# Optimization experiments

Measured on AMD Instinct MI355X. Metric: run time of the kernel, lower is better.

Reference implementation:

```python
import jax, jax.numpy as jnp
import numpy as np

B, C, N, D, K, M, E, G = 2, 64, 16384, 3, 128, 1, 262144, 3


def setup_inputs() -> dict:
    key = jax.random.key(0)
    ks = jax.random.split(key, 15)
    scale = 1.0 / (C * C)
    return {
        "x": jax.random.normal(ks[0], (B, C, N), jnp.float32),
        "nodes": jax.random.uniform(ks[1], (B, N, D), jnp.float32),
        "node_weights": jax.random.uniform(ks[2], (B, N, M), jnp.float32),
        "geo": jax.random.normal(ks[3], (B, G, N), jnp.float32),
        "directed_edges": jax.random.randint(ks[4], (B, E, 2), 0, N, jnp.int32),
        "edge_gradient_weights": 0.1 * jax.random.normal(ks[5], (B, E, D), jnp.float32),
        "modes": jax.random.normal(ks[6], (K, D, M), jnp.float32),
        "weights_c": scale * jax.random.uniform(ks[7], (C, C, K, M), jnp.float32),
        "weights_s": scale * jax.random.uniform(ks[8], (C, C, K, M), jnp.float32),
        "weights_0": scale * jax.random.uniform(ks[9], (C, C, 1, M), jnp.float32),
        "W": jax.random.normal(ks[10], (C, C), jnp.float32) / np.sqrt(C),
        "gw": jax.random.normal(ks[11], (C, C * D), jnp.float32) / np.sqrt(C * D),
        "geo_wx": jax.random.normal(ks[12], (C, G), jnp.float32) / np.sqrt(G),
        "wx": jax.random.normal(ks[13], (C, C), jnp.float32) / np.sqrt(C),
        "w2": jax.random.normal(ks[14], (C, C), jnp.float32) / np.sqrt(C),
    }


def reference(x, nodes, node_weights, geo, directed_edges, edge_gradient_weights,
              modes, weights_c, weights_s, weights_0, W, gw, geo_wx, wx, w2):
    # ---- Fourier bases: cos(kx), sin(kx), 1 -------------------------------
    temp = jnp.einsum('bxd,kdw->bxkw', nodes, modes)          # [B,N,K,M]
    bases_c, bases_s = jnp.cos(temp), jnp.sin(temp)
    b, n = temp.shape[0], temp.shape[1]
    bases_0 = jnp.ones((b, n, 1, temp.shape[3]), temp.dtype)
    nw = node_weights[:, :, None, :]                          # quadrature weights
    wb_c, wb_s, wb_0 = bases_c * nw, bases_s * nw, bases_0 * nw

    # ---- Spectral convolution (non-uniform Fourier neural layer) ----------
    x_c = jnp.einsum('bix,bxkw->bikw', x, wb_c)
    x_s = -jnp.einsum('bix,bxkw->bikw', x, wb_s)
    x_0 = jnp.einsum('bix,bxkw->bikw', x, wb_0)
    f_c = jnp.einsum('bikw,iokw->bokw', x_c, weights_c) - jnp.einsum('bikw,iokw->bokw', x_s, weights_s)
    f_s = jnp.einsum('bikw,iokw->bokw', x_s, weights_c) + jnp.einsum('bikw,iokw->bokw', x_c, weights_s)
    f_0 = jnp.einsum('bikw,iokw->bokw', x_0, weights_0)
    x1 = (jnp.einsum('bokw,bxkw->box', f_0, bases_0)
          + 2.0 * jnp.einsum('bokw,bxkw->box', f_c, bases_c)
          - 2.0 * jnp.einsum('bokw,bxkw->box', f_s, bases_s))

    # ---- Pointwise linear W ----------------------------------------------
    x2 = jnp.einsum('oi,bix->box', W, x)

    # ---- Least-squares gradient via edge gather + scatter-add -------------
    fT = jnp.transpose(x, (0, 2, 1))                          # [B,N,C]
    tgt, src = directed_edges[..., 0], directed_edges[..., 1]  # [B,E]
    f_src = jnp.take_along_axis(fT, src[:, :, None], axis=1)   # [B,E,C]
    f_tgt = jnp.take_along_axis(fT, tgt[:, :, None], axis=1)
    df = f_src - f_tgt
    # message[b,e,c,d] = w[b,e,d] * df[b,e,c], flattened c-major -> [B,E,C*D]
    msg = (df[..., :, None] * edge_gradient_weights[..., None, :]).reshape(b, tgt.shape[1], -1)
    gradf = jnp.zeros((b, n, msg.shape[-1]), msg.dtype).at[jnp.arange(b)[:, None], tgt].add(msg)
    x3 = jnp.einsum('og,bng->bon', gw, gradf)                  # [B,C,N]

    # ---- Geo embedding: w2 @ (softsign(geo_wx@geo) * (wx@x)) --------------
    h = jax.nn.soft_sign(jnp.einsum('og,bgx->box', geo_wx, geo)) * jnp.einsum('oi,bix->box', wx, x)
    x4 = jnp.einsum('oi,bix->box', w2, h)

    return jax.nn.gelu(x1 + x2 + x3 + x4, approximate=False)
```

## Files before the change

kernel.cpp:

```cpp
#include <hip/hip_runtime.h>
#include <hip/hip_fp16.h>
#include <math.h>

#define BB 2
#define CC 64
#define NN 16384
#define DD 3
#define KK 128
#define EE 262144
#define GG 3
#define PP 128
#define LL (NN/PP)
#define KTOT 576

typedef short bf16x8 __attribute__((ext_vector_type(8)));
typedef float f32x4  __attribute__((ext_vector_type(4)));

__device__ __forceinline__ short f2bf(float f) {
    unsigned u = __float_as_uint(f);
    u += 0x7FFF + ((u >> 16) & 1);
    return (short)(u >> 16);
}
__device__ __forceinline__ float bf2f(unsigned short u) {
    return __uint_as_float(((unsigned)u) << 16);
}

constexpr size_t OFF_XB   = 0;
constexpr size_t OFF_PC   = OFF_XB   + (size_t)BB*NN*32;
constexpr size_t OFF_PS   = OFF_PC   + (size_t)BB*PP*CC*KK;
constexpr size_t OFF_BIN4 = OFF_PC;
constexpr size_t OFF_AC   = OFF_PS   + (size_t)BB*PP*CC*KK;
constexpr size_t OFF_AS   = OFF_AC   + (size_t)BB*CC*KK;
constexpr size_t OFF_F0   = OFF_AS   + (size_t)BB*CC*KK;
constexpr size_t OFF_X0   = OFF_F0   + (size_t)BB*CC;
constexpr size_t OFF_CNT  = OFF_X0   + (size_t)BB*CC;
constexpr size_t OFF_OFFS = OFF_CNT  + (size_t)BB*NN;
constexpr size_t OFF_RANK = OFF_OFFS + (size_t)BB*NN;
constexpr size_t OFF_GRB  = OFF_RANK + (size_t)BB*EE;
constexpr size_t OFF_APAN = OFF_GRB  + (size_t)BB*NN*96;
constexpr size_t OFF_GWXT = OFF_APAN + (size_t)BB*KTOT*CC/2;

#define S_A0 (BB*(NN/64))
#define S_A1 (S_A0 + BB*CC)
#define S_A2 (S_A1 + (BB*EE)/256)
#define S_A3 (S_A2 + 48)
#define S_A4 (S_A3 + BB*PP*4)
__global__ void __launch_bounds__(256) k1(const float* __restrict__ x,
                                          const float* __restrict__ nwt,
                                          const int* __restrict__ edges,
                                          const float* __restrict__ W,
                                          const float* __restrict__ gw,
                                          const float* __restrict__ geo_wx,
                                          const float* __restrict__ w2,
                                          const float* __restrict__ nodes,
                                          const float* __restrict__ modes,
                                          unsigned short* __restrict__ xB,
                                          float* __restrict__ x0,
                                          int* __restrict__ counts,
                                          int* __restrict__ rank,
                                          float* __restrict__ gwxT,
                                          short* __restrict__ ApanB,
                                          float* __restrict__ pc,
                                          float* __restrict__ ps) {
    int blk = blockIdx.x;
    int tid = threadIdx.x;
    __shared__ __align__(16) char smem[36864];
    if (blk < S_A0) {
        float (*tile)[65] = (float (*)[65])smem;
        int b = blk / (NN/64);
        int n0 = (blk % (NN/64)) * 64;
        int c = tid & 63, r4 = tid >> 6;
        for (int rr = 0; rr < 16; rr++) {
            int i = r4*16 + rr;
            tile[i][c] = x[((size_t)b*CC + i)*NN + n0 + c];
        }
        __syncthreads();
        for (int rr = 0; rr < 16; rr++) {
            int nn = r4*16 + rr;
            xB[((size_t)b*NN + n0 + nn)*64 + c] = (unsigned short)f2bf(tile[c][nn]);
        }
    } else if (blk < S_A1) {
        float* red = (float*)smem;
        int bi = blk - S_A0;
        int b = bi >> 6, i = bi & 63;
        const float4* __restrict__ xr = (const float4*)&x[((size_t)b*CC + i)*NN];
        const float4* __restrict__ wr = (const float4*)&nwt[(size_t)b*NN];
        float s = 0.f;
        for (int t = tid; t < NN/4; t += 256) {
            float4 xv = xr[t];
            float4 wv = wr[t];
            s += xv.x*wv.x + xv.y*wv.y + xv.z*wv.z + xv.w*wv.w;
        }
        red[tid] = s;
        __syncthreads();
        for (int off = 128; off > 0; off >>= 1) {
            if (tid < off) red[tid] += red[tid+off];
            __syncthreads();
        }
        if (tid == 0) x0[b*CC + i] = red[0];
    } else if (blk < S_A2) {
        int idx = (blk - S_A1)*256 + tid;
        int tgt = edges[(size_t)idx*2 + 0];
        int b = idx / EE;
        rank[idx] = atomicAdd(&counts[b*NN + tgt], 1);
    } else if (blk < S_A3) {
        int idx = (blk - S_A2)*256 + tid;
        if (idx < CC*CC) {
            int j = idx>>6, o = idx&63;
            short wv  = f2bf(W[o*CC+j]);
            short w2v = f2bf(w2[o*CC+j]);
            ApanB[((size_t)(0*CC+o))*KTOT + 256 + j] = wv;
            ApanB[((size_t)(1*CC+o))*KTOT + 256 + j] = wv;
            ApanB[((size_t)(0*CC+o))*KTOT + 320 + j] = w2v;
            ApanB[((size_t)(1*CC+o))*KTOT + 320 + j] = w2v;
        }
        if (idx < CC*CC*DD) {
            int g = idx>>6, o = idx&63;
            short gv = f2bf(gw[o*(CC*DD)+g]);
            ApanB[((size_t)(0*CC+o))*KTOT + 384 + g] = gv;
            ApanB[((size_t)(1*CC+o))*KTOT + 384 + g] = gv;
        }
        if (idx < GG*CC) { int g = idx>>6, i = idx&63; gwxT[idx] = geo_wx[i*GG+g]; }
    } else {
        short* Axw = (short*)smem;
        short* Bc  = (short*)(smem + 17408);
        short* Bsn = (short*)(smem + 17408 + 8704);
        float* ndl = (float*)(smem + 17408 + 8704 + 8704);
        int bc = blk - S_A3;
        int b = bc >> 9;
        int rem = bc & 511;
        int chunk = rem >> 2;
        int kt = rem & 3;
        int k0 = kt * 32;
        int nbase = chunk * LL;
        int lane = tid & 63;
        int w = tid >> 6;
        int col = lane & 15;
        int quad = lane >> 4;
        int wk = w & 1;
        int wi = w >> 1;

        for (int e = tid; e < LL*3; e += 256) ndl[e] = nodes[((size_t)b*NN + nbase)*3 + e];
#pragma unroll
        for (int s = 0; s < 8; s++) {
            int e = tid + s*256;
            int i = e >> 5, seg = e & 31;
            float4 xv = *(const float4*)&x[((size_t)b*CC + i)*NN + nbase + seg*4];
            float4 wv = *(const float4*)&nwt[(size_t)b*NN + nbase + seg*4];
            unsigned lo = (unsigned)(unsigned short)f2bf(xv.x*wv.x)
                        | ((unsigned)(unsigned short)f2bf(xv.y*wv.y) << 16);
            unsigned hi = (unsigned)(unsigned short)f2bf(xv.z*wv.z)
                        | ((unsigned)(unsigned short)f2bf(xv.w*wv.w) << 16);
            *(uint2*)&Axw[i*136 + seg*4] = make_uint2(lo, hi);
        }
        __syncthreads();
#pragma unroll
        for (int s = 0; s < 16; s++) {
            int e = tid + s*256;
            int n = e & 127, kl = e >> 7;
            int k = k0 + kl;
            float t = ndl[n*3+0]*modes[k*3+0] + ndl[n*3+1]*modes[k*3+1]
                    + ndl[n*3+2]*modes[k*3+2];
            Bc [kl*136 + n] = f2bf(__cosf(t));
            Bsn[kl*136 + n] = f2bf(__sinf(t));
        }
        __syncthreads();

        f32x4 ac[2], as4[2];
#pragma unroll
        for (int it = 0; it < 2; it++)
#pragma unroll
            for (int r = 0; r < 4; r++) { ac[it][r] = 0.f; as4[it][r] = 0.f; }

        int rowB = (wk*16 + col)*136;
#pragma unroll
        for (int ns = 0; ns < 4; ns++) {
            int koff = ns*32 + quad*8;
            bf16x8 bcf = *(bf16x8*)&Bc [rowB + koff];
            bf16x8 bsf = *(bf16x8*)&Bsn[rowB + koff];
#pragma unroll
            for (int it = 0; it < 2; it++) {
                int itile = wi*2 + it;
                bf16x8 af = *(bf16x8*)&Axw[(itile*16 + col)*136 + koff];
                ac[it]  = __builtin_amdgcn_mfma_f32_16x16x32_bf16(af, bcf, ac[it], 0, 0, 0);
                as4[it] = __builtin_amdgcn_mfma_f32_16x16x32_bf16(af, bsf, as4[it], 0, 0, 0);
            }
        }
        int base = (b*PP + chunk)*CC;
        int kw = k0 + wk*16 + col;
#pragma unroll
        for (int it = 0; it < 2; it++) {
#pragma unroll
            for (int r = 0; r < 4; r++) {
                int i = (wi*2 + it)*16 + quad*4 + r;
                pc[(size_t)(base + i)*KK + kw] = ac[it][r];
                ps[(size_t)(base + i)*KK + kw] = as4[it][r];
            }
        }
    }
}

__global__ void __launch_bounds__(256) k2(const float* __restrict__ pc, const float* __restrict__ ps,
                                          float* __restrict__ Ac, float* __restrict__ As,
                                          const int* __restrict__ counts,
                                          int* __restrict__ offsets) {
    int blk = blockIdx.x;
    int tid = threadIdx.x;
    if (blk < 256) {
        int idx = blk*64 + (tid >> 2);
        int sub = tid & 3;
        if (idx >= BB*CC*KK) return;
        int b = idx / (CC*KK);
        int r = idx % (CC*KK);
        float sc = 0.f, ss = 0.f;
        for (int ch = sub; ch < PP; ch += 4) {
            size_t o = ((size_t)(b*PP + ch)*CC)*KK + r;
            sc += pc[o]; ss += ps[o];
        }
        sc += __shfl_xor(sc, 1); sc += __shfl_xor(sc, 2);
        ss += __shfl_xor(ss, 1); ss += __shfl_xor(ss, 2);
        if (sub == 0) { Ac[idx] = sc; As[idx] = ss; }
    } else {
        int b = blk - 256;
        __shared__ int part[256];
        int base = b*NN + tid*64;
        int s = 0;
        for (int j = 0; j < 64; j++) s += counts[base + j];
        part[tid] = s;
        __syncthreads();
        for (int off = 1; off < 256; off <<= 1) {
            int v = (tid >= off) ? part[tid - off] : 0;
            __syncthreads();
            part[tid] += v;
            __syncthreads();
        }
        int excl = part[tid] - s;
        for (int j = 0; j < 64; j++) {
            int c = counts[base + j];
            offsets[base + j] = excl;
            excl += c;
        }
    }
}

__global__ void __launch_bounds__(256) k3(const float* __restrict__ Ac, const float* __restrict__ As_,
                                          const float* __restrict__ wc, const float* __restrict__ wsw,
                                          const float* __restrict__ w0, const float* __restrict__ x0,
                                          const int* __restrict__ edges, const float* __restrict__ egw,
                                          const int* __restrict__ offs, const int* __restrict__ rank,
                                          float4* __restrict__ bin4,
                                          short* __restrict__ ApanB, float* __restrict__ f0) {
    int idx = blockIdx.x;
    int tid = threadIdx.x;
    if (idx >= BB*CC*2) {
        int e = (idx - BB*CC*2)*256 + tid;
        int b = e / EE;
        int tgt = edges[(size_t)e*2+0];
        int src = edges[(size_t)e*2+1];
        const float* __restrict__ ew = &egw[(size_t)e*3];
        float e0 = ew[0], e1 = ew[1], e2 = ew[2];
        int pos = offs[b*NN+tgt] + rank[e];
        bin4[(size_t)b*EE + pos] = make_float4(__int_as_float(src), e0, e1, e2);
        return;
    }
    int b = idx / (CC*2);
    int rem = idx % (CC*2);
    int o = rem >> 1, khalf = rem & 1;
    int kl = tid & 63, ig = tid >> 6;
    int k = khalf*64 + kl;
    float fc = 0.f, fs = 0.f;
    for (int ii = 0; ii < 16; ii++) {
        int i = ig*16 + ii;
        float a_c = Ac[(b*CC+i)*KK + k];
        float a_s = As_[(b*CC+i)*KK + k];
        float wcc = wc[((size_t)(i*CC+o))*KK + k];
        float wss = wsw[((size_t)(i*CC+o))*KK + k];
        fc += a_c*wcc + a_s*wss;
        fs += a_c*wss - a_s*wcc;
    }
    __shared__ float rc[256], rs[256];
    __shared__ float f0s[64];
    rc[tid] = fc; rs[tid] = fs;
    if (khalf == 0 && tid < 64) f0s[tid] = x0[b*CC + tid] * w0[tid*CC + o];
    __syncthreads();
    if (ig == 0) {
        fc = rc[kl] + rc[64+kl] + rc[128+kl] + rc[192+kl];
        fs = rs[kl] + rs[64+kl] + rs[128+kl] + rs[192+kl];
        unsigned pk = (unsigned)(unsigned short)f2bf(2.f*fc)
                    | ((unsigned)(unsigned short)f2bf(-2.f*fs) << 16);
        ((unsigned*)ApanB)[((size_t)(b*CC + o))*(KTOT/2) + k] = pk;
    }
    if (khalf == 0 && tid == 0) {
        float acc = 0.f;
        for (int i = 0; i < 64; i++) acc += f0s[i];
        f0[b*CC+o] = acc;
    }
}

#define ECAP2 512
__global__ void __launch_bounds__(256) k_eg(const unsigned short* __restrict__ xB,
                                            const int* __restrict__ offsets,
                                            const float4* __restrict__ bin4,
                                            const float* __restrict__ nodes,
                                            const float* __restrict__ modes,
                                            const float* __restrict__ geo,
                                            const short* __restrict__ ApanB,
                                            const float* __restrict__ f0,
                                            const float* __restrict__ wx,
                                            const float* __restrict__ gwxT,
                                            float* __restrict__ out) {
    int blk = blockIdx.x;
    int b  = blk >> 8;
    int n0 = (blk & 255) * 64;
    int tid = threadIdx.x;
    int lane = tid & 63;
    int w = tid >> 6;
    int w16 = w * 16;
    int col  = lane & 15;
    int quad = lane >> 4;
    int quad8 = quad * 8;
    int quad4 = quad * 4;

    __shared__ __align__(16) char smem[56832];
    short* As = (short*)smem;
    short* Bs = (short*)(smem + 9216);
    short* Ws = (short*)(smem + 18432);
    float4* ebuf = (float4*)smem;
    int* soff = (int*)(smem + 8192);
    unsigned short* gradfL = (unsigned short*)(smem + 27648);
    float* ndl  = (float*)(smem + 55296);
    float* geo3 = (float*)(smem + 56064);

    if (tid < 192) ndl[tid]  = nodes[((size_t)b*NN + n0)*3 + tid];
    if (tid < 192) geo3[tid] = geo[((size_t)b*GG + (tid >> 6))*NN + n0 + (tid & 63)];
    if (tid < 65)  soff[tid] = (n0 + tid < NN) ? offsets[b*NN + n0 + tid] : EE;
    __syncthreads();

    const unsigned short* __restrict__ xBb = xB + (size_t)b*NN*64 + lane;
    for (int r = 0; r < 4; r++) {
        int nb = r*16;
        int base = soff[nb];
        int end  = soff[nb+16];
        float a0[4], a1[4], a2[4], s0[4], s1[4], s2[4];
#pragma unroll
        for (int q = 0; q < 4; q++) { a0[q]=a1[q]=a2[q]=0.f; s0[q]=s1[q]=s2[q]=0.f; }
        for (int cs = base; cs < end; cs += ECAP2) {
            int ce = min(cs + ECAP2, end);
            __syncthreads();
            for (int t = cs + tid; t < ce; t += 256)
                ebuf[t - cs] = bin4[(size_t)b*EE + t];
            __syncthreads();
#pragma unroll
            for (int q = 0; q < 4; q++) {
                int nl = nb + w*4 + q;
                int js = max(soff[nl], cs);
                int je = min(soff[nl+1], ce);
#pragma unroll 4
                for (int j = js; j < je; j++) {
                    float4 e = ebuf[j - cs];
                    int src = __float_as_int(e.x);
                    float xs = bf2f(xBb[(size_t)src*64]);
                    a0[q] = fmaf(xs, e.y, a0[q]);
                    a1[q] = fmaf(xs, e.z, a1[q]);
                    a2[q] = fmaf(xs, e.w, a2[q]);
                    s0[q] += e.y; s1[q] += e.z; s2[q] += e.w;
                }
            }
        }
#pragma unroll
        for (int q = 0; q < 4; q++) {
            int nl = nb + w*4 + q;
            float xtgt = bf2f(xBb[(size_t)(n0 + nl)*64]);
            float fv0 = a0[q] - xtgt*s0[q];
            float fv1 = a1[q] - xtgt*s1[q];
            float fv2 = a2[q] - xtgt*s2[q];
            int g0 = lane*3;
            gradfL[(g0>>6)*4608 + nl*72 + (g0&63)] = (unsigned short)f2bf(fv0);
            int g1 = g0+1;
            gradfL[(g1>>6)*4608 + nl*72 + (g1&63)] = (unsigned short)f2bf(fv1);
            int g2 = g0+2;
            gradfL[(g2>>6)*4608 + nl*72 + (g2&63)] = (unsigned short)f2bf(fv2);
        }
    }
    __syncthreads();

    for (int e = tid; e < 4096; e += 256) {
        int i = e >> 6, j = e & 63;
        Ws[i*72 + j] = f2bf(wx[i*64 + j]);
    }
    f32x4 acc[4], xwa[4];
    float f0v[4];
#pragma unroll
    for (int r = 0; r < 4; r++) f0v[r] = f0[b*CC + w16 + quad4 + r];
#pragma unroll
    for (int nt = 0; nt < 4; nt++) {
#pragma unroll
        for (int r = 0; r < 4; r++) { acc[nt][r] = f0v[r]; xwa[nt][r] = 0.f; }
    }

    const short* __restrict__ Ab = ApanB + ((size_t)b*CC)*KTOT;

    for (int c = 0; c < 9; c++) {
        __syncthreads();
        for (int e = tid; e < 512; e += 256) {
            int o = e >> 3, seg = e & 7;
            *(uint4*)&As[o*72 + seg*8] =
                *(const uint4*)&Ab[(size_t)o*KTOT + c*64 + seg*8];
        }
        if (c < 4) {
#pragma unroll
            for (int s = 0; s < 8; s++) {
                int e = tid + s*256;
                int n = e >> 5, kpl = e & 31;
                int kp = c*32 + kpl;
                float t = ndl[n*3+0]*modes[kp*3+0] + ndl[n*3+1]*modes[kp*3+1]
                        + ndl[n*3+2]*modes[kp*3+2];
                unsigned pk = (unsigned)(unsigned short)f2bf(__cosf(t))
                            | ((unsigned)(unsigned short)f2bf(__sinf(t)) << 16);
                ((unsigned*)Bs)[n*36 + kpl] = pk;
            }
        } else if (c == 4) {
            for (int e = tid; e < 512; e += 256) {
                int n = e >> 3, seg = e & 7;
                *(uint4*)&Bs[n*72 + seg*8] =
                    *(const uint4*)&xB[((size_t)(b*NN + n0 + n))*64 + seg*8];
            }
        } else if (c == 5) {
#pragma unroll
            for (int r = 0; r < 4; r++) {
                int i = w16 + quad4 + r;
                float g0 = gwxT[i], g1 = gwxT[64+i], g2 = gwxT[128+i];
#pragma unroll
                for (int nt = 0; nt < 4; nt++) {
                    int n = nt*16 + col;
                    float t = g0*geo3[n] + g1*geo3[64+n] + g2*geo3[128+n];
                    float ssv = t / (1.f + fabsf(t));
                    Bs[n*72 + i] = f2bf(ssv * xwa[nt][r]);
                }
            }
        }
        __syncthreads();
        const short* Bbase = (c >= 6) ? (const short*)&gradfL[(size_t)(c-6)*4608] : Bs;
        int rowA = (w16 + col) * 72;
#pragma unroll
        for (int ko = 0; ko < 2; ko++) {
            int koff = ko*32 + quad8;
            bf16x8 af = *(bf16x8*)&As[rowA + koff];
            if (c == 4) {
                bf16x8 wf = *(bf16x8*)&Ws[rowA + koff];
#pragma unroll
                for (int nt = 0; nt < 4; nt++) {
                    bf16x8 bfv = *(bf16x8*)&Bbase[(nt*16 + col)*72 + koff];
                    acc[nt] = __builtin_amdgcn_mfma_f32_16x16x32_bf16(af, bfv, acc[nt], 0, 0, 0);
                    xwa[nt] = __builtin_amdgcn_mfma_f32_16x16x32_bf16(wf, bfv, xwa[nt], 0, 0, 0);
                }
            } else {
#pragma unroll
                for (int nt = 0; nt < 4; nt++) {
                    bf16x8 bfv = *(bf16x8*)&Bbase[(nt*16 + col)*72 + koff];
                    acc[nt] = __builtin_amdgcn_mfma_f32_16x16x32_bf16(af, bfv, acc[nt], 0, 0, 0);
                }
            }
        }
    }
#pragma unroll
    for (int nt = 0; nt < 4; nt++) {
#pragma unroll
        for (int r = 0; r < 4; r++) {
            int o = w16 + quad4 + r;
            float v = acc[nt][r];
            float g = 0.5f * v * (1.f + erff(v * 0.70710678118654752f));
            out[((size_t)b*CC + o)*NN + n0 + nt*16 + col] = g;
        }
    }
}

extern "C" void kernel_launch(void* const* d_in, const int* in_sizes, int n_in,
                              void* d_out, int out_size, void* d_ws, size_t ws_size,
                              hipStream_t stream) {
    const float* x      = (const float*)d_in[0];
    const float* nodes  = (const float*)d_in[1];
    const float* nwt    = (const float*)d_in[2];
    const float* geo    = (const float*)d_in[3];
    const int*   edges  = (const int*)d_in[4];
    const float* egw    = (const float*)d_in[5];
    const float* modes  = (const float*)d_in[6];
    const float* wc     = (const float*)d_in[7];
    const float* wsw    = (const float*)d_in[8];
    const float* w0     = (const float*)d_in[9];
    const float* W      = (const float*)d_in[10];
    const float* gw     = (const float*)d_in[11];
    const float* geo_wx = (const float*)d_in[12];
    const float* wx     = (const float*)d_in[13];
    const float* w2     = (const float*)d_in[14];

    float* ws   = (float*)d_ws;
    unsigned short* xB  = (unsigned short*)(ws + OFF_XB);
    float* pc   = ws + OFF_PC;
    float* ps   = ws + OFF_PS;
    float* Ac   = ws + OFF_AC;
    float* As_  = ws + OFF_AS;
    float* f0   = ws + OFF_F0;
    float* x0   = ws + OFF_X0;
    int*  counts = (int*)(ws + OFF_CNT);
    int*  offs   = (int*)(ws + OFF_OFFS);
    int*  rank   = (int*)(ws + OFF_RANK);
    float4* bin4 = (float4*)(ws + OFF_BIN4);
    short* ApanB  = (short*)(ws + OFF_APAN);
    float* gwxT   = ws + OFF_GWXT;
    float* out  = (float*)d_out;

    hipMemsetAsync(counts, 0, (size_t)(BB*NN)*sizeof(int), stream);

    k1 <<<S_A4, 256, 0, stream>>>(x, nwt, edges, W, gw, geo_wx, w2, nodes, modes,
                                  xB, x0, counts, rank, gwxT, ApanB, pc, ps);
    k2 <<<256 + BB, 256, 0, stream>>>(pc, ps, Ac, As_, counts, offs);
    k3 <<<BB*CC*2 + (BB*EE)/256, 256, 0, stream>>>(Ac, As_, wc, wsw, w0, x0,
                                                   edges, egw, offs, rank, bin4, ApanB, f0);
    k_eg <<<BB*(NN/64), 256, 0, stream>>>(xB, offs, bin4, nodes, modes, geo,
                                          ApanB, f0, wx, gwxT, out);
}
```

Baseline: 208.3 us.

## Halve node tile in k_eg and read edge records directly from global

The fused edge-gradient/GEMM kernel now handles 32 nodes per block instead of 64. That doubles the grid and cuts LDS use to roughly 37.8 KB, which should allow more resident blocks. The edge gather no longer stages edge records through shared memory in chunks; each wave reads its nodes' float4 edge records straight from global memory. This removes the per-chunk __syncthreads barriers. The cost is more redundant per-block work: the A panel loads and the wx-to-bf16 conversion now repeat for twice as many blocks, and each wave issues uncoalesced broadcast global loads for edge data.

```diff
diff --git a/kernel.cpp b/kernel.cpp
--- a/kernel.cpp
+++ b/kernel.cpp
@@ -297,7 +297,6 @@
     }
 }
 
-#define ECAP2 512
 __global__ void __launch_bounds__(256) k_eg(const unsigned short* __restrict__ xB,
                                             const int* __restrict__ offsets,
                                             const float4* __restrict__ bin4,
@@ -310,8 +309,8 @@
                                             const float* __restrict__ gwxT,
                                             float* __restrict__ out) {
     int blk = blockIdx.x;
-    int b  = blk >> 8;
-    int n0 = (blk & 255) * 64;
+    int b  = blk >> 9;
+    int n0 = (blk & 511) * 32;
     int tid = threadIdx.x;
     int lane = tid & 63;
     int w = tid >> 6;
@@ -321,79 +320,61 @@
     int quad8 = quad * 8;
     int quad4 = quad * 4;
 
-    __shared__ __align__(16) char smem[56832];
+    __shared__ __align__(16) char smem[37776];
     short* As = (short*)smem;
     short* Bs = (short*)(smem + 9216);
-    short* Ws = (short*)(smem + 18432);
-    float4* ebuf = (float4*)smem;
-    int* soff = (int*)(smem + 8192);
-    unsigned short* gradfL = (unsigned short*)(smem + 27648);
-    float* ndl  = (float*)(smem + 55296);
-    float* geo3 = (float*)(smem + 56064);
-
-    if (tid < 192) ndl[tid]  = nodes[((size_t)b*NN + n0)*3 + tid];
-    if (tid < 192) geo3[tid] = geo[((size_t)b*GG + (tid >> 6))*NN + n0 + (tid & 63)];
-    if (tid < 65)  soff[tid] = (n0 + tid < NN) ? offsets[b*NN + n0 + tid] : EE;
+    short* Ws = (short*)(smem + 13824);
+    unsigned short* gradfL = (unsigned short*)(smem + 23040);
+    float* ndl  = (float*)(smem + 36864);
+    float* geo3 = (float*)(smem + 37248);
+    int* soff   = (int*)(smem + 37632);
+
+    if (tid < 96) ndl[tid]  = nodes[((size_t)b*NN + n0)*3 + tid];
+    if (tid < 96) geo3[tid] = geo[((size_t)b*GG + (tid >> 5))*NN + n0 + (tid & 31)];
+    if (tid < 33) {
+        int idx = n0 + tid;
+        soff[tid] = (idx < NN) ? offsets[b*NN + idx] : EE;
+    }
     __syncthreads();
 
     const unsigned short* __restrict__ xBb = xB + (size_t)b*NN*64 + lane;
-    for (int r = 0; r < 4; r++) {
-        int nb = r*16;
-        int base = soff[nb];
-        int end  = soff[nb+16];
-        float a0[4], a1[4], a2[4], s0[4], s1[4], s2[4];
-#pragma unroll
-        for (int q = 0; q < 4; q++) { a0[q]=a1[q]=a2[q]=0.f; s0[q]=s1[q]=s2[q]=0.f; }
-        for (int cs = base; cs < end; cs += ECAP2) {
-            int ce = min(cs + ECAP2, end);
-            __syncthreads();
-            for (int t = cs + tid; t < ce; t += 256)
-                ebuf[t - cs] = bin4[(size_t)b*EE + t];
-            __syncthreads();
-#pragma unroll
-            for (int q = 0; q < 4; q++) {
-                int nl = nb + w*4 + q;
-                int js = max(soff[nl], cs);
-                int je = min(soff[nl+1], ce);
+    const float4* __restrict__ binb = bin4 + (size_t)b*EE;
+    for (int q = 0; q < 8; q++) {
+        int nl = w*8 + q;
+        int js = soff[nl], je = soff[nl+1];
+        float a0 = 0.f, a1 = 0.f, a2 = 0.f, s0 = 0.f, s1 = 0.f, s2 = 0.f;
 #pragma unroll 4
-                for (int j = js; j < je; j++) {
-                    float4 e = ebuf[j - cs];
-                    int src = __float_as_int(e.x);
-                    float xs = bf2f(xBb[(size_t)src*64]);
-                    a0[q] = fmaf(xs, e.y, a0[q]);
-                    a1[q] = fmaf(xs, e.z, a1[q]);
-                    a2[q] = fmaf(xs, e.w, a2[q]);
-                    s0[q] += e.y; s1[q] += e.z; s2[q] += e.w;
-                }
-            }
-        }
-#pragma unroll
-        for (int q = 0; q < 4; q++) {
-            int nl = nb + w*4 + q;
-            float xtgt = bf2f(xBb[(size_t)(n0 + nl)*64]);
-            float fv0 = a0[q] - xtgt*s0[q];
-            float fv1 = a1[q] - xtgt*s1[q];
-            float fv2 = a2[q] - xtgt*s2[q];
-            int g0 = lane*3;
-            gradfL[(g0>>6)*4608 + nl*72 + (g0&63)] = (unsigned short)f2bf(fv0);
-            int g1 = g0+1;
-            gradfL[(g1>>6)*4608 + nl*72 + (g1&63)] = (unsigned short)f2bf(fv1);
-            int g2 = g0+2;
-            gradfL[(g2>>6)*4608 + nl*72 + (g2&63)] = (unsigned short)f2bf(fv2);
-        }
-    }
-    __syncthreads();
+        for (int j = js; j < je; j++) {
+            float4 e = binb[j];
+            int src = __float_as_int(e.x);
+            float xs = bf2f(xBb[(size_t)src*64]);
+            a0 = fmaf(xs, e.y, a0);
+            a1 = fmaf(xs, e.z, a1);
+            a2 = fmaf(xs, e.w, a2);
+            s0 += e.y; s1 += e.z; s2 += e.w;
+        }
+        float xtgt = bf2f(xBb[(size_t)(n0 + nl)*64]);
+        float fv0 = a0 - xtgt*s0;
+        float fv1 = a1 - xtgt*s1;
+        float fv2 = a2 - xtgt*s2;
+        int g0 = lane*3;
+        gradfL[(g0>>6)*2304 + nl*72 + (g0&63)] = (unsigned short)f2bf(fv0);
+        int g1 = g0 + 1;
+        gradfL[(g1>>6)*2304 + nl*72 + (g1&63)] = (unsigned short)f2bf(fv1);
+        int g2 = g0 + 2;
+        gradfL[(g2>>6)*2304 + nl*72 + (g2&63)] = (unsigned short)f2bf(fv2);
+    }
 
     for (int e = tid; e < 4096; e += 256) {
         int i = e >> 6, j = e & 63;
         Ws[i*72 + j] = f2bf(wx[i*64 + j]);
     }
-    f32x4 acc[4], xwa[4];
+    f32x4 acc[2], xwa[2];
     float f0v[4];
 #pragma unroll
     for (int r = 0; r < 4; r++) f0v[r] = f0[b*CC + w16 + quad4 + r];
 #pragma unroll
-    for (int nt = 0; nt < 4; nt++) {
+    for (int nt = 0; nt < 2; nt++) {
 #pragma unroll
         for (int r = 0; r < 4; r++) { acc[nt][r] = f0v[r]; xwa[nt][r] = 0.f; }
     }
@@ -409,7 +390,7 @@
         }
         if (c < 4) {
 #pragma unroll
-            for (int s = 0; s < 8; s++) {
+            for (int s = 0; s < 4; s++) {
                 int e = tid + s*256;
                 int n = e >> 5, kpl = e & 31;
                 int kp = c*32 + kpl;
@@ -420,7 +401,8 @@
                 ((unsigned*)Bs)[n*36 + kpl] = pk;
             }
         } else if (c == 4) {
-            for (int e = tid; e < 512; e += 256) {
+            {
+                int e = tid;
                 int n = e >> 3, seg = e & 7;
                 *(uint4*)&Bs[n*72 + seg*8] =
                     *(const uint4*)&xB[((size_t)(b*NN + n0 + n))*64 + seg*8];
@@ -431,16 +413,16 @@
                 int i = w16 + quad4 + r;
                 float g0 = gwxT[i], g1 = gwxT[64+i], g2 = gwxT[128+i];
 #pragma unroll
-                for (int nt = 0; nt < 4; nt++) {
+                for (int nt = 0; nt < 2; nt++) {
                     int n = nt*16 + col;
-                    float t = g0*geo3[n] + g1*geo3[64+n] + g2*geo3[128+n];
+                    float t = g0*geo3[n] + g1*geo3[32+n] + g2*geo3[64+n];
                     float ssv = t / (1.f + fabsf(t));
                     Bs[n*72 + i] = f2bf(ssv * xwa[nt][r]);
                 }
             }
         }
         __syncthreads();
-        const short* Bbase = (c >= 6) ? (const short*)&gradfL[(size_t)(c-6)*4608] : Bs;
+        const short* Bbase = (c >= 6) ? (const short*)&gradfL[(size_t)(c-6)*2304] : Bs;
         int rowA = (w16 + col) * 72;
 #pragma unroll
         for (int ko = 0; ko < 2; ko++) {
@@ -449,14 +431,14 @@
             if (c == 4) {
                 bf16x8 wf = *(bf16x8*)&Ws[rowA + koff];
 #pragma unroll
-                for (int nt = 0; nt < 4; nt++) {
+                for (int nt = 0; nt < 2; nt++) {
                     bf16x8 bfv = *(bf16x8*)&Bbase[(nt*16 + col)*72 + koff];
                     acc[nt] = __builtin_amdgcn_mfma_f32_16x16x32_bf16(af, bfv, acc[nt], 0, 0, 0);
                     xwa[nt] = __builtin_amdgcn_mfma_f32_16x16x32_bf16(wf, bfv, xwa[nt], 0, 0, 0);
                 }
             } else {
 #pragma unroll
-                for (int nt = 0; nt < 4; nt++) {
+                for (int nt = 0; nt < 2; nt++) {
                     bf16x8 bfv = *(bf16x8*)&Bbase[(nt*16 + col)*72 + koff];
                     acc[nt] = __builtin_amdgcn_mfma_f32_16x16x32_bf16(af, bfv, acc[nt], 0, 0, 0);
                 }
@@ -464,7 +446,7 @@
         }
     }
 #pragma unroll
-    for (int nt = 0; nt < 4; nt++) {
+    for (int nt = 0; nt < 2; nt++) {
 #pragma unroll
         for (int r = 0; r < 4; r++) {
             int o = w16 + quad4 + r;
@@ -517,6 +499,6 @@
     k2 <<<256 + BB, 256, 0, stream>>>(pc, ps, Ac, As_, counts, offs);
     k3 <<<BB*CC*2 + (BB*EE)/256, 256, 0, stream>>>(Ac, As_, wc, wsw, w0, x0,
                                                    edges, egw, offs, rank, bin4, ApanB, f0);
-    k_eg <<<BB*(NN/64), 256, 0, stream>>>(xB, offs, bin4, nodes, modes, geo,
+    k_eg <<<BB*(NN/32), 256, 0, stream>>>(xB, offs, bin4, nodes, modes, geo,
                                           ApanB, f0, wx, gwxT, out);
 }
```

New measurement: 199.6 us. 4.2% less time.
